# Kernel optimization log

Measured on AMD Instinct MI355X. Metric: run time of the kernel, lower is better.

Reference implementation:

```python
import jax, jax.numpy as jnp
import numpy as np

D = 2048
N_HID = 512
ATT = 512
BATCH = 256
L = 196


def setup_inputs() -> dict:
    key = jax.random.key(0)
    ks = jax.random.split(key, 8)
    s = 0.02
    return {
        "feature": jax.random.normal(ks[0], (BATCH, L, D), dtype=jnp.float32),
        "prev_h": jax.random.normal(ks[1], (BATCH, N_HID), dtype=jnp.float32),
        "W_enc": jax.random.normal(ks[2], (D, ATT), dtype=jnp.float32) * s,
        "b_enc": jnp.zeros((ATT,), dtype=jnp.float32),
        "W_dec": jax.random.normal(ks[3], (N_HID, ATT), dtype=jnp.float32) * s,
        "b_dec": jnp.zeros((ATT,), dtype=jnp.float32),
        "W_tot": jax.random.normal(ks[4], (ATT, 1), dtype=jnp.float32) * s,
        "b_tot": jnp.zeros((1,), dtype=jnp.float32),
    }


def reference(feature, prev_h, W_enc, b_enc, W_dec, b_dec, W_tot, b_tot):
    # att1: (N, L, A); att2: (N, A)
    att1 = jnp.einsum("nld,da->nla", feature, W_enc) + b_enc
    att2 = prev_h @ W_dec + b_dec
    att = jax.nn.relu(att1 + att2[:, None, :])          # (N, L, A)
    scores = (att @ W_tot)[..., 0] + b_tot[0]           # (N, L)
    alpha = jax.nn.softmax(scores, axis=1)              # (N, L)
    weighted_feature = jnp.einsum("nld,nl->nd", feature, alpha)  # (N, D)
    return weighted_feature, alpha
```

## Files before the change

### kernel.cpp

```cpp
#include <hip/hip_runtime.h>
#include <hip/hip_bf16.h>


typedef unsigned short u16;
typedef __attribute__((ext_vector_type(8))) short short8;
typedef __attribute__((ext_vector_type(4))) float f32x4;

#define BATCH 256
#define LQ    196
#define DDIM  2048
#define ADIM  512
#define MTOT  (BATCH * LQ)
#define WF_N  (BATCH * DDIM)
#define KQP   1032

__device__ __forceinline__ u16 f2bf(float f) {
  unsigned u = __builtin_bit_cast(unsigned, f);
  return (u16)((u + 0x7FFFu + ((u >> 16) & 1u)) >> 16);
}

__device__ __forceinline__ ushort4 cvt4(float4 f) {
  ushort4 r;
  r.x = f2bf(f.x); r.y = f2bf(f.y); r.z = f2bf(f.z); r.w = f2bf(f.w);
  return r;
}

__device__ __forceinline__ void glds16(const u16* g, u16* l) {
  __builtin_amdgcn_global_load_lds(
      (const __attribute__((address_space(1))) unsigned int*)g,
      (__attribute__((address_space(3))) unsigned int*)l, 16, 0, 0);
}

__global__ void prepB_k(const float* __restrict__ W_enc, u16* __restrict__ Bst) {
  const int ks = blockIdx.x;
  const int tid = threadIdx.x;
  __shared__ u16 ldsT[32 * 520];
  for (int i4 = tid; i4 < 4096; i4 += 256) {
    int dl = i4 >> 7;
    int nn = (i4 & 127) << 2;
    float4 f = *(const float4*)(W_enc + (size_t)(ks * 32 + dl) * 512 + nn);
    *(ushort4*)(&ldsT[dl * 520 + nn]) = cvt4(f);
  }
  __syncthreads();
  for (int idx = tid; idx < 16384; idx += 256) {
    int kq = idx >> 12;
    int n  = (idx >> 3) & 511;
    int e  = idx & 7;
    Bst[(size_t)ks * 16384 + idx] = ldsT[(kq * 8 + e) * 520 + n];
  }
}

__global__ void att2_k(const float* __restrict__ prev_h,
                       const float* __restrict__ W_dec,
                       const float* __restrict__ b_dec,
                       const float* __restrict__ b_enc,
                       float* __restrict__ att2) {
  const int n = blockIdx.x, tid = threadIdx.x;
  __shared__ float ph[512];
  ph[tid]       = prev_h[n * 512 + tid];
  ph[tid + 256] = prev_h[n * 512 + tid + 256];
  __syncthreads();
  float a0 = b_dec[tid] + b_enc[tid];
  float a1 = b_dec[tid + 256] + b_enc[tid + 256];
  #pragma unroll 8
  for (int h = 0; h < 512; h++) {
    float p = ph[h];
    a0 = fmaf(p, W_dec[h * 512 + tid], a0);
    a1 = fmaf(p, W_dec[h * 512 + tid + 256], a1);
  }
  att2[n * 512 + tid] = a0;
  att2[n * 512 + tid + 256] = a1;
}

__global__ void zero_scores_k(float* __restrict__ s) {
  s[blockIdx.x * 256 + threadIdx.x] = 0.f;
}

__global__ __launch_bounds__(256, 3) void score_gemm_k(
    const float* __restrict__ feature, const u16* __restrict__ Bst,
    const float* __restrict__ att2, const float* __restrict__ W_tot,
    float* __restrict__ scores) {
  __shared__ __align__(16) u16 sA[2][4 * KQP];
  __shared__ __align__(16) u16 sB[2][4 * KQP];
  __shared__ float sRed[2][128];

  const int tid = threadIdx.x;
  const int b = blockIdx.x;
  const int mt = (b >> 5) * 8 + (b & 7);
  const int nt = (b >> 3) & 3;
  const int r0 = mt << 7, n0 = nt << 7;
  const int wid = tid >> 6, lane = tid & 63;
  const int wgm = wid >> 1, wgn = wid & 1;
  const int quad = lane >> 4, cid = lane & 15;

  const int arow = tid >> 3, akk4 = tid & 7;
  const float* gA = feature + (size_t)(r0 + arow) * 2048 + akk4 * 4;
  const int wAoff = (akk4 >> 1) * KQP + (arow << 3) + ((akk4 & 1) << 2);

  const u16* gBlane = Bst + (size_t)wid * 4096 + ((size_t)n0 << 3) + lane * 8;

  const int abase = quad * KQP + (((wgm << 6) + cid) << 3);
  const int bbase = quad * KQP + (((wgn << 6) + cid) << 3);

  f32x4 zero = {0.f, 0.f, 0.f, 0.f};
  f32x4 acc[4][4];
  #pragma unroll
  for (int i = 0; i < 4; i++)
    #pragma unroll
    for (int j = 0; j < 4; j++) acc[i][j] = zero;

  float4 a0, a1, a2, a3;
  {
    const float* p = gA;
    a0 = *(const float4*)(p);
    a1 = *(const float4*)(p + 32 * 2048);
    a2 = *(const float4*)(p + 64 * 2048);
    a3 = *(const float4*)(p + 96 * 2048);
    u16* dst = &sB[0][wid * KQP];
    glds16(gBlane, dst);
    glds16(gBlane + 512, dst + 512);
  }

  for (int ks = 0; ks < 64; ks++) {
    const int buf = ks & 1;
    u16* wa = &sA[buf][wAoff];
    *(ushort4*)(wa)       = cvt4(a0);
    *(ushort4*)(wa + 256) = cvt4(a1);
    *(ushort4*)(wa + 512) = cvt4(a2);
    *(ushort4*)(wa + 768) = cvt4(a3);
    __syncthreads();

    if (ks < 63) {
      const float* p = gA + (ks + 1) * 32;
      a0 = *(const float4*)(p);
      a1 = *(const float4*)(p + 32 * 2048);
      a2 = *(const float4*)(p + 64 * 2048);
      a3 = *(const float4*)(p + 96 * 2048);
      const u16* src = gBlane + (size_t)(ks + 1) * 16384;
      u16* dst = &sB[buf ^ 1][wid * KQP];
      glds16(src, dst);
      glds16(src + 512, dst + 512);
    }

    const u16* sa = &sA[buf][abase];
    const u16* sb = &sB[buf][bbase];
    short8 af[4], bfr[4];
    #pragma unroll
    for (int mi = 0; mi < 4; mi++)
      af[mi] = *(const short8*)(sa + (mi << 7));
    #pragma unroll
    for (int ni = 0; ni < 4; ni++)
      bfr[ni] = *(const short8*)(sb + (ni << 7));
    #pragma unroll
    for (int mi = 0; mi < 4; mi++)
      #pragma unroll
      for (int ni = 0; ni < 4; ni++)
        acc[mi][ni] = __builtin_amdgcn_mfma_f32_16x16x32_bf16(
            af[mi], bfr[ni], acc[mi][ni], 0, 0, 0);
  }

  float wt[4];
  #pragma unroll
  for (int ni = 0; ni < 4; ni++)
    wt[ni] = W_tot[n0 + (wgn << 6) + ni * 16 + cid];

  #pragma unroll
  for (int mi = 0; mi < 4; mi++) {
    #pragma unroll
    for (int reg = 0; reg < 4; reg++) {
      int row_local = (wgm << 6) + mi * 16 + quad * 4 + reg;
      int row_flat = r0 + row_local;
      int nb = row_flat / 196;
      const float* a2r = att2 + nb * 512 + n0 + (wgn << 6);
      float s = 0.f;
      #pragma unroll
      for (int ni = 0; ni < 4; ni++) {
        float v = acc[mi][ni][reg] + a2r[ni * 16 + cid];
        s += fmaxf(v, 0.f) * wt[ni];
      }
      s += __shfl_xor(s, 1); s += __shfl_xor(s, 2);
      s += __shfl_xor(s, 4); s += __shfl_xor(s, 8);
      if (cid == 0) sRed[wgn][row_local] = s;
    }
  }
  __syncthreads();
  if (tid < 128) atomicAdd(&scores[r0 + tid], sRed[0][tid] + sRed[1][tid]);
}

__global__ void softmax_k(const float* __restrict__ scores,
                          float* __restrict__ alpha) {
  const int n = blockIdx.x, tid = threadIdx.x;
  __shared__ float red[8];
  float s = (tid < LQ) ? scores[n * LQ + tid] : -1e30f;
  float m = s;
  for (int o = 32; o; o >>= 1) m = fmaxf(m, __shfl_xor(m, o));
  if ((tid & 63) == 0) red[tid >> 6] = m;
  __syncthreads();
  m = fmaxf(fmaxf(red[0], red[1]), fmaxf(red[2], red[3]));
  float e = (tid < LQ) ? __expf(s - m) : 0.f;
  float t = e;
  for (int o = 32; o; o >>= 1) t += __shfl_xor(t, o);
  if ((tid & 63) == 0) red[4 + (tid >> 6)] = t;
  __syncthreads();
  t = red[4] + red[5] + red[6] + red[7];
  if (tid < LQ) alpha[n * LQ + tid] = e / t;
}

__global__ void wsum_k(const float* __restrict__ feature,
                       const float* __restrict__ alpha,
                       float* __restrict__ out) {
  const int n = blockIdx.x >> 1, half = blockIdx.x & 1;
  const int tid = threadIdx.x;
  __shared__ float al[LQ];
  if (tid < LQ) al[tid] = alpha[n * LQ + tid];
  __syncthreads();
  const float* fp = feature + (size_t)n * LQ * DDIM + half * 1024 + tid * 4;
  float4 acc = {0.f, 0.f, 0.f, 0.f};
  #pragma unroll 4
  for (int l = 0; l < LQ; l++) {
    float a = al[l];
    float4 f = *(const float4*)(fp + (size_t)l * DDIM);
    acc.x = fmaf(a, f.x, acc.x); acc.y = fmaf(a, f.y, acc.y);
    acc.z = fmaf(a, f.z, acc.z); acc.w = fmaf(a, f.w, acc.w);
  }
  *(float4*)(out + n * DDIM + half * 1024 + tid * 4) = acc;
}

extern "C" void kernel_launch(void* const* d_in, const int* in_sizes, int n_in,
                              void* d_out, int out_size, void* d_ws, size_t ws_size,
                              hipStream_t stream) {
  const float* feature = (const float*)d_in[0];
  const float* prev_h  = (const float*)d_in[1];
  const float* W_enc   = (const float*)d_in[2];
  const float* b_enc   = (const float*)d_in[3];
  const float* W_dec   = (const float*)d_in[4];
  const float* b_dec   = (const float*)d_in[5];
  const float* W_tot   = (const float*)d_in[6];

  float* out   = (float*)d_out;
  float* wf    = out;
  float* alpha = out + WF_N;

  char* ws = (char*)d_ws;
  u16*   Bst    = (u16*)ws;
  float* att2   = (float*)(ws + (2u << 20));
  float* scores = (float*)(ws + (2u << 20) + (512u << 10));

  prepB_k<<<64, 256, 0, stream>>>(W_enc, Bst);
  att2_k<<<256, 256, 0, stream>>>(prev_h, W_dec, b_dec, b_enc, att2);
  zero_scores_k<<<196, 256, 0, stream>>>(scores);
  score_gemm_k<<<1568, 256, 0, stream>>>(feature, Bst, att2, W_tot, scores);
  softmax_k<<<256, 256, 0, stream>>>(scores, alpha);
  wsum_k<<<512, 256, 0, stream>>>(feature, alpha, wf);
}
```

Measured before the change: 773.8 us.

## Merge prep kernels, use native bf16 convert, raise GEMM occupancy and wsum unroll

Folds the weight-transpose, att2 and score-zeroing kernels into one launch, with att2 split into two blocks per batch row. This removes two launch gaps and gives the att2 step more parallelism. It also swaps the manual round-to-nearest bf16 conversion for the compiler's __bf16 cast, raises the score GEMM's launch-bounds target from 3 to 4 blocks per SM, and doubles the unroll in the weighted-sum loop. The higher occupancy target may force register spills in the MFMA kernel.

```diff
diff --git a/kernel.cpp b/kernel.cpp
--- a/kernel.cpp
+++ b/kernel.cpp
@@ -14,14 +14,12 @@
 #define WF_N  (BATCH * DDIM)
 #define KQP   1032
 
-__device__ __forceinline__ u16 f2bf(float f) {
-  unsigned u = __builtin_bit_cast(unsigned, f);
-  return (u16)((u + 0x7FFFu + ((u >> 16) & 1u)) >> 16);
-}
-
 __device__ __forceinline__ ushort4 cvt4(float4 f) {
   ushort4 r;
-  r.x = f2bf(f.x); r.y = f2bf(f.y); r.z = f2bf(f.z); r.w = f2bf(f.w);
+  r.x = __builtin_bit_cast(u16, (__bf16)f.x);
+  r.y = __builtin_bit_cast(u16, (__bf16)f.y);
+  r.z = __builtin_bit_cast(u16, (__bf16)f.z);
+  r.w = __builtin_bit_cast(u16, (__bf16)f.w);
   return r;
 }
 
@@ -31,52 +29,48 @@
       (__attribute__((address_space(3))) unsigned int*)l, 16, 0, 0);
 }
 
-__global__ void prepB_k(const float* __restrict__ W_enc, u16* __restrict__ Bst) {
-  const int ks = blockIdx.x;
-  const int tid = threadIdx.x;
-  __shared__ u16 ldsT[32 * 520];
-  for (int i4 = tid; i4 < 4096; i4 += 256) {
-    int dl = i4 >> 7;
-    int nn = (i4 & 127) << 2;
-    float4 f = *(const float4*)(W_enc + (size_t)(ks * 32 + dl) * 512 + nn);
-    *(ushort4*)(&ldsT[dl * 520 + nn]) = cvt4(f);
-  }
-  __syncthreads();
-  for (int idx = tid; idx < 16384; idx += 256) {
-    int kq = idx >> 12;
-    int n  = (idx >> 3) & 511;
-    int e  = idx & 7;
-    Bst[(size_t)ks * 16384 + idx] = ldsT[(kq * 8 + e) * 520 + n];
-  }
-}
-
-__global__ void att2_k(const float* __restrict__ prev_h,
+__global__ void prep_k(const float* __restrict__ W_enc, u16* __restrict__ Bst,
+                       const float* __restrict__ prev_h,
                        const float* __restrict__ W_dec,
                        const float* __restrict__ b_dec,
                        const float* __restrict__ b_enc,
-                       float* __restrict__ att2) {
-  const int n = blockIdx.x, tid = threadIdx.x;
-  __shared__ float ph[512];
-  ph[tid]       = prev_h[n * 512 + tid];
-  ph[tid + 256] = prev_h[n * 512 + tid + 256];
-  __syncthreads();
-  float a0 = b_dec[tid] + b_enc[tid];
-  float a1 = b_dec[tid + 256] + b_enc[tid + 256];
-  #pragma unroll 8
-  for (int h = 0; h < 512; h++) {
-    float p = ph[h];
-    a0 = fmaf(p, W_dec[h * 512 + tid], a0);
-    a1 = fmaf(p, W_dec[h * 512 + tid + 256], a1);
-  }
-  att2[n * 512 + tid] = a0;
-  att2[n * 512 + tid + 256] = a1;
-}
-
-__global__ void zero_scores_k(float* __restrict__ s) {
-  s[blockIdx.x * 256 + threadIdx.x] = 0.f;
-}
-
-__global__ __launch_bounds__(256, 3) void score_gemm_k(
+                       float* __restrict__ att2,
+                       float* __restrict__ scores) {
+  const int b = blockIdx.x, tid = threadIdx.x;
+  __shared__ u16 smem[32 * 520];
+  if (b < 64) {
+    const int ks = b;
+    for (int i4 = tid; i4 < 4096; i4 += 256) {
+      int dl = i4 >> 7;
+      int nn = (i4 & 127) << 2;
+      float4 f = *(const float4*)(W_enc + (size_t)(ks * 32 + dl) * 512 + nn);
+      *(ushort4*)(&smem[dl * 520 + nn]) = cvt4(f);
+    }
+    __syncthreads();
+    for (int idx = tid; idx < 16384; idx += 256) {
+      int kq = idx >> 12;
+      int n  = (idx >> 3) & 511;
+      int e  = idx & 7;
+      Bst[(size_t)ks * 16384 + idx] = smem[(kq * 8 + e) * 520 + n];
+    }
+  } else if (b < 576) {
+    const int n  = (b - 64) >> 1;
+    const int c0 = ((b - 64) & 1) << 8;
+    float* ph = (float*)smem;
+    ph[tid]       = prev_h[n * 512 + tid];
+    ph[tid + 256] = prev_h[n * 512 + tid + 256];
+    __syncthreads();
+    float a0 = b_dec[c0 + tid] + b_enc[c0 + tid];
+    #pragma unroll 8
+    for (int h = 0; h < 512; h++)
+      a0 = fmaf(ph[h], W_dec[h * 512 + c0 + tid], a0);
+    att2[n * 512 + c0 + tid] = a0;
+  } else {
+    scores[(b - 576) * 256 + tid] = 0.f;
+  }
+}
+
+__global__ __launch_bounds__(256, 4) void score_gemm_k(
     const float* __restrict__ feature, const u16* __restrict__ Bst,
     const float* __restrict__ att2, const float* __restrict__ W_tot,
     float* __restrict__ scores) {
@@ -216,7 +210,7 @@
   __syncthreads();
   const float* fp = feature + (size_t)n * LQ * DDIM + half * 1024 + tid * 4;
   float4 acc = {0.f, 0.f, 0.f, 0.f};
-  #pragma unroll 4
+  #pragma unroll 8
   for (int l = 0; l < LQ; l++) {
     float a = al[l];
     float4 f = *(const float4*)(fp + (size_t)l * DDIM);
@@ -246,9 +240,8 @@
   float* att2   = (float*)(ws + (2u << 20));
   float* scores = (float*)(ws + (2u << 20) + (512u << 10));
 
-  prepB_k<<<64, 256, 0, stream>>>(W_enc, Bst);
-  att2_k<<<256, 256, 0, stream>>>(prev_h, W_dec, b_dec, b_enc, att2);
-  zero_scores_k<<<196, 256, 0, stream>>>(scores);
+  prep_k<<<772, 256, 0, stream>>>(W_enc, Bst, prev_h, W_dec, b_dec, b_enc,
+                                  att2, scores);
   score_gemm_k<<<1568, 256, 0, stream>>>(feature, Bst, att2, W_tot, scores);
   softmax_k<<<256, 256, 0, stream>>>(scores, alpha);
   wsum_k<<<512, 256, 0, stream>>>(feature, alpha, wf);
```

Result: faster. 751.5 us (-2.9%).
